# Performance work log

Measured on AMD Instinct MI355X. Metric: run time of the kernel, lower is better.

The kernel has to match this reference:

```python
import jax, jax.numpy as jnp
import numpy as np


def setup_inputs() -> dict:
    key = jax.random.key(0)
    ks = jax.random.split(key, 8)
    C, dk = 256, 32
    B, H, W = 4, 64, 64
    x = jax.random.normal(ks[0], (B, C, H, W), dtype=jnp.float32)
    wq = jax.random.normal(ks[1], (dk, C), dtype=jnp.float32) * (1.0 / np.sqrt(C))
    bq = jnp.zeros((dk,), dtype=jnp.float32)
    wk = jax.random.normal(ks[2], (dk, C), dtype=jnp.float32) * (1.0 / np.sqrt(C))
    bk = jnp.zeros((dk,), dtype=jnp.float32)
    wv = jax.random.normal(ks[3], (C, C), dtype=jnp.float32) * (1.0 / np.sqrt(C))
    bv = jnp.zeros((C,), dtype=jnp.float32)
    gamma = jnp.ones((1,), dtype=jnp.float32)
    return {"x": x, "wq": wq, "bq": bq, "wk": wk, "bk": bk,
            "wv": wv, "bv": bv, "gamma": gamma}


def reference(x, wq, bq, wk, bk, wv, bv, gamma):
    B, C, H, W = x.shape
    N = H * W
    xf = x.reshape(B, C, N)  # [B, C, N]
    # 1x1 convs == per-pixel linear projections
    q = jnp.einsum('dc,bcn->bnd', wq, xf) + bq  # [B, N, dk]  (proj_query, permuted)
    k = jnp.einsum('dc,bcn->bdn', wk, xf) + bk[None, :, None]  # [B, dk, N]
    v = jnp.einsum('ec,bcn->ben', wv, xf) + bv[None, :, None]  # [B, C, N]
    energy = jnp.einsum('bnd,bdm->bnm', q, k)  # [B, N, N]
    attention = jax.nn.softmax(energy, axis=-1)
    # out[b,c,i] = sum_j v[b,c,j] * attention[b,i,j]
    out = jnp.einsum('bcj,bij->bci', v, attention)  # [B, C, N]
    out = out.reshape(B, C, H, W)
    return gamma[0] * out + x
```

## Files before the change

kernel.cpp:

```cpp
#include <hip/hip_runtime.h>
#include <hip/hip_bf16.h>

#define NPIX 4096
#define CIN  256
#define DK   32

typedef __attribute__((ext_vector_type(8))) short short8;
typedef __attribute__((ext_vector_type(16))) float f32x16;

__device__ __forceinline__ unsigned short f2bf(float f) {
    unsigned int u = __float_as_uint(f);
    return (unsigned short)((u + 0x7fffu + ((u >> 16) & 1u)) >> 16);
}
__device__ __forceinline__ float bf2f(unsigned short h) {
    return __uint_as_float(((unsigned int)h) << 16);
}
__device__ __forceinline__ unsigned int f2bf2(float a, float b) {
    __hip_bfloat162 h = __float22bfloat162_rn(make_float2(a, b));
    unsigned int u;
    __builtin_memcpy(&u, &h, 4);
    return u;
}

__global__ void wprep_kernel(const float* __restrict__ wq, const float* __restrict__ wk,
                             const float* __restrict__ wv,
                             unsigned short* __restrict__ wqh, unsigned short* __restrict__ wql,
                             unsigned short* __restrict__ wkh, unsigned short* __restrict__ wkl,
                             unsigned short* __restrict__ wvh) {
    const int lane = threadIdx.x & 63, li = lane & 31, hi = lane >> 5;
    const int kc = blockIdx.x, y = blockIdx.y;
    if (y < 4) {
        const float* m = (y < 2) ? wq : wk;
        short8 h8, l8;
#pragma unroll
        for (int e = 0; e < 8; ++e) {
            float v = m[li * CIN + kc * 16 + hi * 8 + e];
            unsigned short hb = f2bf(v);
            h8[e] = (short)hb;
            l8[e] = (short)f2bf(v - bf2f(hb));
        }
        unsigned short* dst = (y == 0) ? wqh : (y == 1) ? wql : (y == 2) ? wkh : wkl;
        *reinterpret_cast<short8*>(&dst[kc * 512 + lane * 8]) = (y & 1) ? l8 : h8;
    } else {
        const int cblk = y - 4;
        short8 h8;
#pragma unroll
        for (int e = 0; e < 8; ++e)
            h8[e] = (short)f2bf(wv[(cblk * 32 + li) * CIN + kc * 16 + hi * 8 + e]);
        *reinterpret_cast<short8*>(&wvh[(cblk * 16 + kc) * 512 + lane * 8]) = h8;
    }
}

__global__ __launch_bounds__(512) void projall_kernel(
        const float* __restrict__ x,
        const unsigned short* __restrict__ wqh, const unsigned short* __restrict__ wql,
        const unsigned short* __restrict__ wkh, const unsigned short* __restrict__ wkl,
        const unsigned short* __restrict__ wvh,
        const float* __restrict__ bq, const float* __restrict__ bk, const float* __restrict__ bv,
        unsigned short* __restrict__ qfrag, unsigned short* __restrict__ kfrag,
        unsigned short* __restrict__ vfrag) {
    __shared__ float xs[64][36];
    __shared__ unsigned short xhf[16 * 512];
    __shared__ unsigned short xlf[16 * 512];
    __shared__ unsigned short ts[2][32][40];

    const int t = threadIdx.x, lane = t & 63, li = lane & 31, hi = lane >> 5, w = t >> 6;
    const int nblk = blockIdx.x, b = blockIdx.y;
    const int n0 = nblk * 32;

    for (int cb = 0; cb < 4; ++cb) {
        {
            int c = t >> 3, n4 = (t & 7) * 4;
            float4 v = *reinterpret_cast<const float4*>(
                &x[(size_t)(b * CIN + cb * 64 + c) * NPIX + n0 + n4]);
            xs[c][n4 + 0] = v.x; xs[c][n4 + 1] = v.y;
            xs[c][n4 + 2] = v.z; xs[c][n4 + 3] = v.w;
        }
        __syncthreads();
        {
            const int kc = w & 3;
            const bool isL = (w >= 4);
            short8 f;
#pragma unroll
            for (int e = 0; e < 8; ++e) {
                float v = xs[kc * 16 + hi * 8 + e][li];
                unsigned short hb = f2bf(v);
                f[e] = isL ? (short)f2bf(v - bf2f(hb)) : (short)hb;
            }
            unsigned short* dst = isL ? xlf : xhf;
            *reinterpret_cast<short8*>(&dst[(cb * 4 + kc) * 512 + lane * 8]) = f;
        }
        __syncthreads();
    }

    if (w < 2) {
        const unsigned short* wh = (w == 0) ? wqh : wkh;
        const unsigned short* wl = (w == 0) ? wql : wkl;
        const float* bias = (w == 0) ? bq : bk;
        f32x16 acc;
#pragma unroll
        for (int r = 0; r < 16; ++r) acc[r] = 0.f;
        for (int kc = 0; kc < 16; ++kc) {
            short8 ah = *reinterpret_cast<const short8*>(&xhf[kc * 512 + lane * 8]);
            short8 al = *reinterpret_cast<const short8*>(&xlf[kc * 512 + lane * 8]);
            short8 whf = *reinterpret_cast<const short8*>(&wh[kc * 512 + lane * 8]);
            short8 wlf = *reinterpret_cast<const short8*>(&wl[kc * 512 + lane * 8]);
            acc = __builtin_amdgcn_mfma_f32_32x32x16_bf16(ah, whf, acc, 0, 0, 0);
            acc = __builtin_amdgcn_mfma_f32_32x32x16_bf16(al, whf, acc, 0, 0, 0);
            acc = __builtin_amdgcn_mfma_f32_32x32x16_bf16(ah, wlf, acc, 0, 0, 0);
        }
        const float bs = bias[li];
#pragma unroll
        for (int r = 0; r < 16; ++r) {
            int row = (r & 3) + 8 * (r >> 2) + 4 * hi;
            ts[w][row][li] = f2bf(acc[r] + bs);
        }
        unsigned short* dstf = (w == 0) ? qfrag : kfrag;
#pragma unroll
        for (int dh = 0; dh < 2; ++dh) {
            short8 f = *reinterpret_cast<const short8*>(&ts[w][li][dh * 16 + hi * 8]);
            *reinterpret_cast<short8*>(
                &dstf[((size_t)(b * 128 + nblk) * 2 + dh) * 512 + lane * 8]) = f;
        }
    } else {
        const int w2 = w - 2;
        const int njob = (w2 < 2) ? 2 : 1;
        for (int jj = 0; jj < njob; ++jj) {
            const int cblk = w2 + jj * 6;
            f32x16 acc;
#pragma unroll
            for (int r = 0; r < 16; ++r) acc[r] = 0.f;
            for (int kc = 0; kc < 16; ++kc) {
                short8 xb = *reinterpret_cast<const short8*>(&xhf[kc * 512 + lane * 8]);
                short8 wf = *reinterpret_cast<const short8*>(&wvh[(cblk * 16 + kc) * 512 + lane * 8]);
                acc = __builtin_amdgcn_mfma_f32_32x32x16_bf16(xb, wf, acc, 0, 0, 0);
            }
            const float bvv = bv[cblk * 32 + li];
#pragma unroll
            for (int g = 0; g < 2; ++g) {
                short8 sv;
#pragma unroll
                for (int e = 0; e < 8; ++e) sv[e] = (short)f2bf(acc[g * 8 + e] + bvv);
                *reinterpret_cast<short8*>(
                    &vfrag[((size_t)(b * 8 + cblk) * 256 + nblk * 2 + g) * 512 + lane * 8]) = sv;
            }
        }
    }
}

__global__ __launch_bounds__(512, 4) void attnv_kernel(
        const unsigned short* __restrict__ qfrag, const unsigned short* __restrict__ kfrag,
        const unsigned short* __restrict__ vfrag, unsigned short* __restrict__ opart,
        float* __restrict__ lpart, float* __restrict__ out) {
    __shared__ unsigned short Ps[4 * 8 * 512];
    __shared__ float sred[2][4][32];

    const int t = threadIdx.x, lane = t & 63, li = lane & 31, hi = lane >> 5, w = t >> 6;
    const int blk = blockIdx.x;
    const int xcd = blk & 7, slot = blk >> 3;
    const int jh = slot & 1, ps = slot >> 1;
    const int b = xcd >> 1;
    const int ipos = (xcd & 1) * 32 + ps;

    if (w < 4) {
        const int sl = w;
        short8 qb[2][2];
#pragma unroll
        for (int it = 0; it < 2; ++it) {
            size_t qoff = ((size_t)(b * 128 + ipos * 2 + it) * 2) * 512 + lane * 8;
            qb[it][0] = *reinterpret_cast<const short8*>(&qfrag[qoff]);
            qb[it][1] = *reinterpret_cast<const short8*>(&qfrag[qoff + 512]);
        }
        float ssum[2] = {0.f, 0.f};

        auto do_E = [&](int s) {
            const int buf = s & 1;
            size_t koff = ((size_t)(b * 128 + jh * 64 + s * 4 + sl) * 2) * 512 + lane * 8;
            short8 k0 = *reinterpret_cast<const short8*>(&kfrag[koff]);
            short8 k1 = *reinterpret_cast<const short8*>(&kfrag[koff + 512]);
#pragma unroll
            for (int it = 0; it < 2; ++it) {
                f32x16 e;
#pragma unroll
                for (int r = 0; r < 16; ++r) e[r] = 0.f;
                e = __builtin_amdgcn_mfma_f32_32x32x16_bf16(k0, qb[it][0], e, 0, 0, 0);
                e = __builtin_amdgcn_mfma_f32_32x32x16_bf16(k1, qb[it][1], e, 0, 0, 0);
#pragma unroll
                for (int g = 0; g < 2; ++g) {
                    float p0 = __expf(e[g * 8 + 0]), p1 = __expf(e[g * 8 + 1]);
                    float p2 = __expf(e[g * 8 + 2]), p3 = __expf(e[g * 8 + 3]);
                    float p4 = __expf(e[g * 8 + 4]), p5 = __expf(e[g * 8 + 5]);
                    float p6 = __expf(e[g * 8 + 6]), p7 = __expf(e[g * 8 + 7]);
                    ssum[it] += ((p0 + p1) + (p2 + p3)) + ((p4 + p5) + (p6 + p7));
                    uint4 pk;
                    pk.x = f2bf2(p0, p1); pk.y = f2bf2(p2, p3);
                    pk.z = f2bf2(p4, p5); pk.w = f2bf2(p6, p7);
                    *reinterpret_cast<uint4*>(
                        &Ps[((it * 2 + buf) * 8 + sl * 2 + g) * 512 + lane * 8]) = pk;
                }
            }
        };

        do_E(0);
        __syncthreads();
#pragma unroll 1
        for (int s = 0; s < 16; ++s) {
            if (s + 1 < 16) do_E(s + 1);
            __syncthreads();
        }
#pragma unroll
        for (int it = 0; it < 2; ++it) {
            ssum[it] += __shfl_xor(ssum[it], 32);
            if (lane < 32) sred[it][sl][li] = ssum[it];
        }
        __syncthreads();
        if (sl == 0 && lane < 32) {
#pragma unroll
            for (int it = 0; it < 2; ++it) {
                float lt = sred[it][0][li] + sred[it][1][li] + sred[it][2][li] + sred[it][3][li];
                lpart[((size_t)jh * 4 + b) * NPIX + ipos * 64 + it * 32 + li] = lt;
            }
        }
    } else {
        const int cq2 = w - 4;
        f32x16 acc00, acc01, acc10, acc11;
#pragma unroll
        for (int r = 0; r < 16; ++r) { acc00[r] = 0.f; acc01[r] = 0.f; acc10[r] = 0.f; acc11[r] = 0.f; }

        __syncthreads();
#pragma unroll 1
        for (int s = 0; s < 16; ++s) {
            const int buf = s & 1;
            size_t vb0 = ((size_t)(b * 8 + cq2 * 2)     * 256 + jh * 128 + s * 8) * 512 + lane * 8;
            size_t vb1 = ((size_t)(b * 8 + cq2 * 2 + 1) * 256 + jh * 128 + s * 8) * 512 + lane * 8;
            const unsigned short* p0 = &Ps[(buf * 8) * 512 + lane * 8];
            const unsigned short* p1 = &Ps[((2 + buf) * 8) * 512 + lane * 8];
#pragma unroll
            for (int kc = 0; kc < 8; ++kc) {
                short8 B0 = *reinterpret_cast<const short8*>(p0 + kc * 512);
                short8 B1 = *reinterpret_cast<const short8*>(p1 + kc * 512);
                short8 v0 = *reinterpret_cast<const short8*>(&vfrag[vb0 + kc * 512]);
                short8 v1 = *reinterpret_cast<const short8*>(&vfrag[vb1 + kc * 512]);
                acc00 = __builtin_amdgcn_mfma_f32_32x32x16_bf16(v0, B0, acc00, 0, 0, 0);
                acc01 = __builtin_amdgcn_mfma_f32_32x32x16_bf16(v0, B1, acc01, 0, 0, 0);
                acc10 = __builtin_amdgcn_mfma_f32_32x32x16_bf16(v1, B0, acc10, 0, 0, 0);
                acc11 = __builtin_amdgcn_mfma_f32_32x32x16_bf16(v1, B1, acc11, 0, 0, 0);
            }
            __syncthreads();
        }
        __syncthreads();

#pragma unroll
        for (int cs = 0; cs < 2; ++cs) {
#pragma unroll
            for (int it = 0; it < 2; ++it) {
                const f32x16& A = (cs == 0) ? (it == 0 ? acc00 : acc01)
                                            : (it == 0 ? acc10 : acc11);
#pragma unroll
                for (int r = 0; r < 16; ++r) {
                    int c = cq2 * 64 + cs * 32 + (r & 3) + 8 * (r >> 2) + 4 * hi;
                    size_t idx = (size_t)(b * CIN + c) * NPIX + ipos * 64 + it * 32 + li;
                    if (jh == 0) out[idx] = A[r];
                    else         opart[idx] = f2bf(A[r]);
                }
            }
        }
    }
}

__global__ __launch_bounds__(256) void merge_kernel(
        const unsigned short* __restrict__ opart, const float* __restrict__ lpart,
        const float* __restrict__ xin, const float* __restrict__ gamma,
        float* __restrict__ out) {
    const size_t idx4 = ((size_t)blockIdx.x * 256 + threadIdx.x) * 4;
    const size_t i  = idx4 & (NPIX - 1);
    const size_t b  = idx4 >> 20;
    float4 o0 = *reinterpret_cast<const float4*>(&out[idx4]);
    float4 xv = *reinterpret_cast<const float4*>(&xin[idx4]);
    float4 l0 = *reinterpret_cast<const float4*>(&lpart[b * NPIX + i]);
    float4 l1 = *reinterpret_cast<const float4*>(&lpart[(4 + b) * NPIX + i]);
    const unsigned short* op = &opart[idx4];
    const float g = gamma[0];
    float4 o;
    o.x = g * (o0.x + bf2f(op[0])) / (l0.x + l1.x) + xv.x;
    o.y = g * (o0.y + bf2f(op[1])) / (l0.y + l1.y) + xv.y;
    o.z = g * (o0.z + bf2f(op[2])) / (l0.z + l1.z) + xv.z;
    o.w = g * (o0.w + bf2f(op[3])) / (l0.w + l1.w) + xv.w;
    *reinterpret_cast<float4*>(&out[idx4]) = o;
}

extern "C" void kernel_launch(void* const* d_in, const int* in_sizes, int n_in,
                              void* d_out, int out_size, void* d_ws, size_t ws_size,
                              hipStream_t stream) {
    const float* x     = (const float*)d_in[0];
    const float* wq    = (const float*)d_in[1];
    const float* bq    = (const float*)d_in[2];
    const float* wk    = (const float*)d_in[3];
    const float* bk    = (const float*)d_in[4];
    const float* wv    = (const float*)d_in[5];
    const float* bv    = (const float*)d_in[6];
    const float* gamma = (const float*)d_in[7];
    float* out = (float*)d_out;

    unsigned short* qf    = (unsigned short*)d_ws;
    unsigned short* kf    = qf + (size_t)524288;
    unsigned short* vf    = kf + (size_t)524288;
    unsigned short* wqh   = vf + (size_t)4194304;
    unsigned short* wql   = wqh + 8192;
    unsigned short* wkh   = wql + 8192;
    unsigned short* wkl   = wkh + 8192;
    unsigned short* wvh   = wkl + 8192;
    unsigned short* opart = wvh + 65536;
    float*          lpart = (float*)(opart + 4194304);

    wprep_kernel<<<dim3(16, 12), 64, 0, stream>>>(wq, wk, wv, wqh, wql, wkh, wkl, wvh);
    projall_kernel<<<dim3(128, 4), 512, 0, stream>>>(x, wqh, wql, wkh, wkl, wvh,
                                                     bq, bk, bv, qf, kf, vf);
    attnv_kernel<<<dim3(512), 512, 0, stream>>>(qf, kf, vf, opart, lpart, out);
    merge_kernel<<<dim3(4096), 256, 0, stream>>>(opart, lpart, x, gamma, out);
}
```

Before: 143.6 us.

## Unify warp roles so every wave computes both exp scores and PV MFMAs

Replaces the warp-specialized split (4 waves computing QK^T/exp, 4 waves doing P·V) with a uniform scheme. Every one of the 8 waves now computes one 32x32 energy tile plus exp for its (it, sl) slot and accumulates a 32-channel slice of the output. K fragments are prefetched two steps ahead and V fragments one step ahead in registers. The intent is to balance MFMA and exp work across all waves and hide global load latency. The cost is more live registers per wave (8 V fragments plus accumulators) under the existing 512-thread, 4-block launch bounds, which may cause spills or lower occupancy.

```diff
diff --git a/kernel.cpp b/kernel.cpp
--- a/kernel.cpp
+++ b/kernel.cpp
@@ -161,109 +161,98 @@
     const int jh = slot & 1, ps = slot >> 1;
     const int b = xcd >> 1;
     const int ipos = (xcd & 1) * 32 + ps;
-
-    if (w < 4) {
-        const int sl = w;
-        short8 qb[2][2];
-#pragma unroll
-        for (int it = 0; it < 2; ++it) {
-            size_t qoff = ((size_t)(b * 128 + ipos * 2 + it) * 2) * 512 + lane * 8;
-            qb[it][0] = *reinterpret_cast<const short8*>(&qfrag[qoff]);
-            qb[it][1] = *reinterpret_cast<const short8*>(&qfrag[qoff + 512]);
-        }
-        float ssum[2] = {0.f, 0.f};
-
-        auto do_E = [&](int s) {
-            const int buf = s & 1;
-            size_t koff = ((size_t)(b * 128 + jh * 64 + s * 4 + sl) * 2) * 512 + lane * 8;
-            short8 k0 = *reinterpret_cast<const short8*>(&kfrag[koff]);
-            short8 k1 = *reinterpret_cast<const short8*>(&kfrag[koff + 512]);
-#pragma unroll
-            for (int it = 0; it < 2; ++it) {
-                f32x16 e;
-#pragma unroll
-                for (int r = 0; r < 16; ++r) e[r] = 0.f;
-                e = __builtin_amdgcn_mfma_f32_32x32x16_bf16(k0, qb[it][0], e, 0, 0, 0);
-                e = __builtin_amdgcn_mfma_f32_32x32x16_bf16(k1, qb[it][1], e, 0, 0, 0);
-#pragma unroll
-                for (int g = 0; g < 2; ++g) {
-                    float p0 = __expf(e[g * 8 + 0]), p1 = __expf(e[g * 8 + 1]);
-                    float p2 = __expf(e[g * 8 + 2]), p3 = __expf(e[g * 8 + 3]);
-                    float p4 = __expf(e[g * 8 + 4]), p5 = __expf(e[g * 8 + 5]);
-                    float p6 = __expf(e[g * 8 + 6]), p7 = __expf(e[g * 8 + 7]);
-                    ssum[it] += ((p0 + p1) + (p2 + p3)) + ((p4 + p5) + (p6 + p7));
-                    uint4 pk;
-                    pk.x = f2bf2(p0, p1); pk.y = f2bf2(p2, p3);
-                    pk.z = f2bf2(p4, p5); pk.w = f2bf2(p6, p7);
-                    *reinterpret_cast<uint4*>(
-                        &Ps[((it * 2 + buf) * 8 + sl * 2 + g) * 512 + lane * 8]) = pk;
-                }
-            }
-        };
-
-        do_E(0);
+    const int it = w >> 2, sl = w & 3;
+    const int cq = w;
+
+    short8 qb0, qb1;
+    {
+        size_t qoff = ((size_t)(b * 128 + ipos * 2 + it) * 2) * 512 + lane * 8;
+        qb0 = *reinterpret_cast<const short8*>(&qfrag[qoff]);
+        qb1 = *reinterpret_cast<const short8*>(&qfrag[qoff + 512]);
+    }
+    float ssum = 0.f;
+
+    f32x16 acc0, acc1;
+#pragma unroll
+    for (int r = 0; r < 16; ++r) { acc0[r] = 0.f; acc1[r] = 0.f; }
+
+    short8 kp0, kp1;
+    short8 vp[8];
+
+    auto kload = [&](int s) {
+        size_t koff = ((size_t)(b * 128 + jh * 64 + s * 4 + sl) * 2) * 512 + lane * 8;
+        kp0 = *reinterpret_cast<const short8*>(&kfrag[koff]);
+        kp1 = *reinterpret_cast<const short8*>(&kfrag[koff + 512]);
+    };
+    auto vload = [&](int s) {
+        size_t vb = ((size_t)(b * 8 + cq) * 256 + jh * 128 + s * 8) * 512 + lane * 8;
+#pragma unroll
+        for (int kc = 0; kc < 8; ++kc)
+            vp[kc] = *reinterpret_cast<const short8*>(&vfrag[vb + kc * 512]);
+    };
+    auto do_E = [&](int s) {
+        f32x16 e;
+#pragma unroll
+        for (int r = 0; r < 16; ++r) e[r] = 0.f;
+        e = __builtin_amdgcn_mfma_f32_32x32x16_bf16(kp0, qb0, e, 0, 0, 0);
+        e = __builtin_amdgcn_mfma_f32_32x32x16_bf16(kp1, qb1, e, 0, 0, 0);
+        const int buf = s & 1;
+#pragma unroll
+        for (int g = 0; g < 2; ++g) {
+            float p0 = __expf(e[g * 8 + 0]), p1 = __expf(e[g * 8 + 1]);
+            float p2 = __expf(e[g * 8 + 2]), p3 = __expf(e[g * 8 + 3]);
+            float p4 = __expf(e[g * 8 + 4]), p5 = __expf(e[g * 8 + 5]);
+            float p6 = __expf(e[g * 8 + 6]), p7 = __expf(e[g * 8 + 7]);
+            ssum += ((p0 + p1) + (p2 + p3)) + ((p4 + p5) + (p6 + p7));
+            uint4 pk;
+            pk.x = f2bf2(p0, p1); pk.y = f2bf2(p2, p3);
+            pk.z = f2bf2(p4, p5); pk.w = f2bf2(p6, p7);
+            *reinterpret_cast<uint4*>(
+                &Ps[((it * 2 + buf) * 8 + sl * 2 + g) * 512 + lane * 8]) = pk;
+        }
+    };
+
+    kload(0);
+    vload(0);
+    do_E(0);
+    kload(1);
+    __syncthreads();
+
+#pragma unroll 1
+    for (int s = 0; s < 16; ++s) {
+        if (s + 1 < 16) {
+            do_E(s + 1);
+            if (s + 2 < 16) kload(s + 2);
+        }
+        const int buf = s & 1;
+#pragma unroll
+        for (int kc = 0; kc < 8; ++kc) {
+            short8 B0 = *reinterpret_cast<const short8*>(&Ps[(buf * 8 + kc) * 512 + lane * 8]);
+            short8 B1 = *reinterpret_cast<const short8*>(&Ps[((2 + buf) * 8 + kc) * 512 + lane * 8]);
+            acc0 = __builtin_amdgcn_mfma_f32_32x32x16_bf16(vp[kc], B0, acc0, 0, 0, 0);
+            acc1 = __builtin_amdgcn_mfma_f32_32x32x16_bf16(vp[kc], B1, acc1, 0, 0, 0);
+        }
+        if (s + 1 < 16) vload(s + 1);
         __syncthreads();
-#pragma unroll 1
-        for (int s = 0; s < 16; ++s) {
-            if (s + 1 < 16) do_E(s + 1);
-            __syncthreads();
-        }
-#pragma unroll
-        for (int it = 0; it < 2; ++it) {
-            ssum[it] += __shfl_xor(ssum[it], 32);
-            if (lane < 32) sred[it][sl][li] = ssum[it];
-        }
-        __syncthreads();
-        if (sl == 0 && lane < 32) {
-#pragma unroll
-            for (int it = 0; it < 2; ++it) {
-                float lt = sred[it][0][li] + sred[it][1][li] + sred[it][2][li] + sred[it][3][li];
-                lpart[((size_t)jh * 4 + b) * NPIX + ipos * 64 + it * 32 + li] = lt;
-            }
-        }
-    } else {
-        const int cq2 = w - 4;
-        f32x16 acc00, acc01, acc10, acc11;
-#pragma unroll
-        for (int r = 0; r < 16; ++r) { acc00[r] = 0.f; acc01[r] = 0.f; acc10[r] = 0.f; acc11[r] = 0.f; }
-
-        __syncthreads();
-#pragma unroll 1
-        for (int s = 0; s < 16; ++s) {
-            const int buf = s & 1;
-            size_t vb0 = ((size_t)(b * 8 + cq2 * 2)     * 256 + jh * 128 + s * 8) * 512 + lane * 8;
-            size_t vb1 = ((size_t)(b * 8 + cq2 * 2 + 1) * 256 + jh * 128 + s * 8) * 512 + lane * 8;
-            const unsigned short* p0 = &Ps[(buf * 8) * 512 + lane * 8];
-            const unsigned short* p1 = &Ps[((2 + buf) * 8) * 512 + lane * 8];
-#pragma unroll
-            for (int kc = 0; kc < 8; ++kc) {
-                short8 B0 = *reinterpret_cast<const short8*>(p0 + kc * 512);
-                short8 B1 = *reinterpret_cast<const short8*>(p1 + kc * 512);
-                short8 v0 = *reinterpret_cast<const short8*>(&vfrag[vb0 + kc * 512]);
-                short8 v1 = *reinterpret_cast<const short8*>(&vfrag[vb1 + kc * 512]);
-                acc00 = __builtin_amdgcn_mfma_f32_32x32x16_bf16(v0, B0, acc00, 0, 0, 0);
-                acc01 = __builtin_amdgcn_mfma_f32_32x32x16_bf16(v0, B1, acc01, 0, 0, 0);
-                acc10 = __builtin_amdgcn_mfma_f32_32x32x16_bf16(v1, B0, acc10, 0, 0, 0);
-                acc11 = __builtin_amdgcn_mfma_f32_32x32x16_bf16(v1, B1, acc11, 0, 0, 0);
-            }
-            __syncthreads();
-        }
-        __syncthreads();
-
-#pragma unroll
-        for (int cs = 0; cs < 2; ++cs) {
-#pragma unroll
-            for (int it = 0; it < 2; ++it) {
-                const f32x16& A = (cs == 0) ? (it == 0 ? acc00 : acc01)
-                                            : (it == 0 ? acc10 : acc11);
-#pragma unroll
-                for (int r = 0; r < 16; ++r) {
-                    int c = cq2 * 64 + cs * 32 + (r & 3) + 8 * (r >> 2) + 4 * hi;
-                    size_t idx = (size_t)(b * CIN + c) * NPIX + ipos * 64 + it * 32 + li;
-                    if (jh == 0) out[idx] = A[r];
-                    else         opart[idx] = f2bf(A[r]);
-                }
-            }
+    }
+
+    ssum += __shfl_xor(ssum, 32);
+    if (lane < 32) sred[it][sl][li] = ssum;
+    __syncthreads();
+    if (sl == 0 && lane < 32) {
+        float lt = sred[it][0][li] + sred[it][1][li] + sred[it][2][li] + sred[it][3][li];
+        lpart[((size_t)jh * 4 + b) * NPIX + ipos * 64 + it * 32 + li] = lt;
+    }
+
+#pragma unroll
+    for (int itt = 0; itt < 2; ++itt) {
+        const f32x16& A = itt ? acc1 : acc0;
+#pragma unroll
+        for (int r = 0; r < 16; ++r) {
+            int c = cq * 32 + (r & 3) + 8 * (r >> 2) + 4 * hi;
+            size_t idx = (size_t)(b * CIN + c) * NPIX + ipos * 64 + itt * 32 + li;
+            if (jh == 0) out[idx] = A[r];
+            else         opart[idx] = f2bf(A[r]);
         }
     }
 }
```

Measured after the change: 140.4 us. 2.3% less time.
